# Performance work log

Hardware: AMD Instinct MI355X
Metric: run time of the kernel (lower is better)

## Reference

```python
import jax, jax.numpy as jnp
import numpy as np

IN_FEATURES = 2048
OUT_FEATURES = 2048
BATCH = 4096


def setup_inputs() -> dict:
    key = jax.random.key(0)
    kx, kw, kb, kp = jax.random.split(key, 4)
    x = jax.random.normal(kx, (BATCH, IN_FEATURES), dtype=jnp.float32)
    weight = jax.random.normal(kw, (OUT_FEATURES, IN_FEATURES), dtype=jnp.float32)
    bias = jax.random.normal(kb, (OUT_FEATURES,), dtype=jnp.float32)
    # torch uses torch.randperm(in_features) at forward time; we fix a permutation here
    indices = jax.random.permutation(kp, IN_FEATURES).astype(jnp.int64)
    return {"x": x, "weight": weight, "bias": bias, "indices": indices}


def reference(x, weight, bias, indices):
    # Original: (x[:, None, :] * weight)[:, :, indices].sum(dim=2) + bias
    # Summing the permuted reduction axis == contracting the permuted operands;
    # we gather both x and weight along the permutation then do a real GEMM,
    # avoiding the huge [B, out, in] intermediate while keeping identical math.
    xp = x[:, indices]            # [B, in]
    wp = weight[:, indices]       # [out, in]
    return jnp.einsum('bi,oi->bo', xp, wp) + bias[None, :]
```

## Files before the change

kernel.cpp:

```cpp
#include <hip/hip_runtime.h>
#include <hip/hip_bf16.h>

#define M_DIM 4096
#define N_DIM 2048
#define K_DIM 2048

#define BM 256
#define BN 128
#define BK 64
#define NT (K_DIM / BK)
#define A_TILE (BM * BK)
#define B_TILE (BN * BK)

typedef __bf16 bf16x8 __attribute__((ext_vector_type(8)));
typedef float f32x4 __attribute__((ext_vector_type(4)));
typedef unsigned short u16x8 __attribute__((ext_vector_type(8)));

__device__ __forceinline__ unsigned short f32_to_bf16_rne(float f) {
  unsigned int u = __float_as_uint(f);
  u += 0x7fffu + ((u >> 16) & 1u);
  return (unsigned short)(u >> 16);
}

__global__ __launch_bounds__(256) void cvt_both(
    const float* __restrict__ x, const float* __restrict__ w,
    unsigned short* __restrict__ out, int xn8, int totn8) {
  int i = blockIdx.x * 256 + threadIdx.x;
  if (i >= totn8) return;
  const float* src = (i < xn8) ? (x + (size_t)i * 8)
                               : (w + (size_t)(i - xn8) * 8);
  f32x4 a = reinterpret_cast<const f32x4*>(src)[0];
  f32x4 b = reinterpret_cast<const f32x4*>(src)[1];
  u16x8 o;
  o[0] = f32_to_bf16_rne(a[0]); o[1] = f32_to_bf16_rne(a[1]);
  o[2] = f32_to_bf16_rne(a[2]); o[3] = f32_to_bf16_rne(a[3]);
  o[4] = f32_to_bf16_rne(b[0]); o[5] = f32_to_bf16_rne(b[1]);
  o[6] = f32_to_bf16_rne(b[2]); o[7] = f32_to_bf16_rne(b[3]);
  reinterpret_cast<u16x8*>(out)[i] = o;
}

__device__ __forceinline__ void gload_lds16(const unsigned short* g, unsigned short* l) {
  __builtin_amdgcn_global_load_lds(
      (const __attribute__((address_space(1))) unsigned int*)g,
      (__attribute__((address_space(3))) unsigned int*)l, 16, 0, 0);
}

#define LD8(p) (*reinterpret_cast<const bf16x8*>(p))

__global__ __launch_bounds__(512, 2) void gemm_8w(
    const unsigned short* __restrict__ A,
    const unsigned short* __restrict__ B,
    const float* __restrict__ bias,
    float* __restrict__ C) {
  __shared__ unsigned short As[3 * A_TILE];
  __shared__ unsigned short Bs[3 * B_TILE];

  const int tid  = threadIdx.x;
  const int lane = tid & 63;
  const int wave = tid >> 6;
  const int wr   = wave >> 1;
  const int wc   = wave & 1;
  const int bn   = blockIdx.x;
  const int bm   = blockIdx.y;

  const int srow   = tid >> 3;
  const int schunk = (tid & 7) ^ (srow & 7);
  const unsigned short* Ag[4];
  const unsigned short* Bg[2];
#pragma unroll
  for (int j = 0; j < 4; ++j)
    Ag[j] = A + (size_t)(bm * BM + j * 64 + srow) * K_DIM + schunk * 8;
#pragma unroll
  for (int j = 0; j < 2; ++j)
    Bg[j] = B + (size_t)(bn * BN + j * 64 + srow) * K_DIM + schunk * 8;

#define STAGE_A01(buf, k0) do { \
    unsigned short* _d = &As[(buf) * A_TILE + tid * 8]; \
    gload_lds16(Ag[0] + (k0), _d); \
    gload_lds16(Ag[1] + (k0), _d + 4096); \
  } while (0)
#define STAGE_A23(buf, k0) do { \
    unsigned short* _d = &As[(buf) * A_TILE + 8192 + tid * 8]; \
    gload_lds16(Ag[2] + (k0), _d); \
    gload_lds16(Ag[3] + (k0), _d + 4096); \
  } while (0)
#define STAGE_B01(buf, k0) do { \
    unsigned short* _d = &Bs[(buf) * B_TILE + tid * 8]; \
    gload_lds16(Bg[0] + (k0), _d); \
    gload_lds16(Bg[1] + (k0), _d + 4096); \
  } while (0)

  const int fr = lane & 15;
  const int qq = lane >> 4;
  const int xr = fr & 7;
  int aoff[4][2], boff[4][2];
#pragma unroll
  for (int mi = 0; mi < 4; ++mi)
#pragma unroll
    for (int kk = 0; kk < 2; ++kk)
      aoff[mi][kk] = ((wr * 64 + mi * 16 + fr) * 8 + ((kk * 4 + qq) ^ xr)) * 8;
#pragma unroll
  for (int ni = 0; ni < 4; ++ni)
#pragma unroll
    for (int kk = 0; kk < 2; ++kk)
      boff[ni][kk] = ((wc * 64 + ni * 16 + fr) * 8 + ((kk * 4 + qq) ^ xr)) * 8;

  const f32x4 z = {0.f, 0.f, 0.f, 0.f};
  f32x4 acc[4][4];
#pragma unroll
  for (int i = 0; i < 4; ++i)
#pragma unroll
    for (int j = 0; j < 4; ++j) acc[i][j] = z;

#define MFMA_ROW(mi, av) do { \
    acc[mi][0] = __builtin_amdgcn_mfma_f32_16x16x32_bf16(av, bv0, acc[mi][0], 0, 0, 0); \
    acc[mi][1] = __builtin_amdgcn_mfma_f32_16x16x32_bf16(av, bv1, acc[mi][1], 0, 0, 0); \
    acc[mi][2] = __builtin_amdgcn_mfma_f32_16x16x32_bf16(av, bv2, acc[mi][2], 0, 0, 0); \
    acc[mi][3] = __builtin_amdgcn_mfma_f32_16x16x32_bf16(av, bv3, acc[mi][3], 0, 0, 0); \
  } while (0)

#define BODY(t_, STG) do { \
    const int b_ = (t_) % 3; \
    const unsigned short* Asb = &As[b_ * A_TILE]; \
    const unsigned short* Bsb = &Bs[b_ * B_TILE]; \
    const int sb_ = ((t_) + 2) % 3; \
    const int sk0_ = ((t_) + 2) * BK; \
    bf16x8 av0, av1, av2, av3, bv0, bv1, bv2, bv3; \
     \
    bv0 = LD8(Bsb + boff[0][0]); bv1 = LD8(Bsb + boff[1][0]); \
    bv2 = LD8(Bsb + boff[2][0]); bv3 = LD8(Bsb + boff[3][0]); \
    av0 = LD8(Asb + aoff[0][0]); av1 = LD8(Asb + aoff[1][0]); \
    if (STG) STAGE_A01(sb_, sk0_); \
    __builtin_amdgcn_s_setprio(1); \
    MFMA_ROW(0, av0); MFMA_ROW(1, av1); \
    __builtin_amdgcn_s_setprio(0); \
    av2 = LD8(Asb + aoff[2][0]); av3 = LD8(Asb + aoff[3][0]); \
    if (STG) STAGE_A23(sb_, sk0_); \
    __builtin_amdgcn_s_setprio(1); \
    MFMA_ROW(2, av2); MFMA_ROW(3, av3); \
    __builtin_amdgcn_s_setprio(0); \
     \
    bv0 = LD8(Bsb + boff[0][1]); bv1 = LD8(Bsb + boff[1][1]); \
    bv2 = LD8(Bsb + boff[2][1]); bv3 = LD8(Bsb + boff[3][1]); \
    av0 = LD8(Asb + aoff[0][1]); av1 = LD8(Asb + aoff[1][1]); \
    if (STG) STAGE_B01(sb_, sk0_); \
    __builtin_amdgcn_s_setprio(1); \
    MFMA_ROW(0, av0); MFMA_ROW(1, av1); \
    __builtin_amdgcn_s_setprio(0); \
    av2 = LD8(Asb + aoff[2][1]); av3 = LD8(Asb + aoff[3][1]); \
    __builtin_amdgcn_s_setprio(1); \
    MFMA_ROW(2, av2); MFMA_ROW(3, av3); \
    __builtin_amdgcn_s_setprio(0); \
  } while (0)

  STAGE_A01(0, 0); STAGE_A23(0, 0); STAGE_B01(0, 0);
  STAGE_A01(1, BK); STAGE_A23(1, BK); STAGE_B01(1, BK);
  asm volatile("s_waitcnt vmcnt(6)" ::: "memory");
  __builtin_amdgcn_s_barrier();
  __builtin_amdgcn_sched_barrier(0);

#pragma unroll 1
  for (int t = 0; t < NT - 2; ++t) {
    BODY(t, 1);
    asm volatile("s_waitcnt vmcnt(6)" ::: "memory");
    __builtin_amdgcn_s_barrier();
    __builtin_amdgcn_sched_barrier(0);
  }
  BODY(NT - 2, 0);
  asm volatile("s_waitcnt vmcnt(0)" ::: "memory");
  __builtin_amdgcn_s_barrier();
  __builtin_amdgcn_sched_barrier(0);
  BODY(NT - 1, 0);

  const int orow0 = bm * BM + wr * 64 + qq * 4;
  const int ocol0 = bn * BN + wc * 64 + fr;
#pragma unroll
  for (int ni = 0; ni < 4; ++ni) {
    const int col = ocol0 + ni * 16;
    const float bv = bias[col];
#pragma unroll
    for (int mi = 0; mi < 4; ++mi) {
      const int row = orow0 + mi * 16;
#pragma unroll
      for (int r = 0; r < 4; ++r)
        C[(size_t)(row + r) * N_DIM + col] = acc[mi][ni][r] + bv;
    }
  }
#undef BODY
#undef MFMA_ROW
#undef STAGE_A01
#undef STAGE_A23
#undef STAGE_B01
}

__global__ __launch_bounds__(256) void gemm_f32_naive(
    const float* __restrict__ X, const float* __restrict__ W,
    const float* __restrict__ bias, float* __restrict__ C) {
  int o = blockIdx.x * 256 + threadIdx.x;
  if (o >= M_DIM * N_DIM) return;
  int m = o / N_DIM, n = o % N_DIM;
  const float* xr = X + (size_t)m * K_DIM;
  const float* wr = W + (size_t)n * K_DIM;
  float s = 0.f;
  for (int k = 0; k < K_DIM; ++k) s += xr[k] * wr[k];
  C[o] = s + bias[n];
}

extern "C" void kernel_launch(void* const* d_in, const int* in_sizes, int n_in,
                              void* d_out, int out_size, void* d_ws, size_t ws_size,
                              hipStream_t stream) {
  const float* x    = (const float*)d_in[0];
  const float* w    = (const float*)d_in[1];
  const float* bias = (const float*)d_in[2];
  float* out = (float*)d_out;

  const size_t x_elems = (size_t)M_DIM * K_DIM;
  const size_t w_elems = (size_t)N_DIM * K_DIM;
  const size_t need = (x_elems + w_elems) * sizeof(unsigned short);

  if (ws_size < need) {
    gemm_f32_naive<<<(M_DIM * N_DIM + 255) / 256, 256, 0, stream>>>(x, w, bias, out);
    return;
  }

  unsigned short* xb = (unsigned short*)d_ws;
  unsigned short* wb = xb + x_elems;

  const int xn8 = (int)(x_elems / 8);
  const int totn8 = (int)((x_elems + w_elems) / 8);
  cvt_both<<<(totn8 + 255) / 256, 256, 0, stream>>>(x, w, xb, xn8, totn8);

  dim3 grid(N_DIM / BN, M_DIM / BM);
  gemm_8w<<<grid, 512, 0, stream>>>(xb, wb, bias, out);
}
```

Measured before the change: 62.09 us.

## Restructure K-loop into two barrier-synchronized load/MFMA phases per tile

Each K-tile iteration is reorganized into two halves. In each half, all LDS fragment reads and global-to-LDS staging are issued first, then the block hits a barrier and waits on lgkmcnt, then 16 MFMAs run back-to-back. This replaces the earlier interleaving of loads and MFMAs within a half. The goal is to keep all waves in lockstep, ping-pong style, so memory and matrix phases from co-resident blocks overlap and MFMA bursts are longer. It adds several extra barriers per tile and removes intra-wave overlap of LDS reads with MFMAs, which risks stalls.

```diff
diff --git a/kernel.cpp b/kernel.cpp
--- a/kernel.cpp
+++ b/kernel.cpp
@@ -119,7 +119,12 @@
     acc[mi][3] = __builtin_amdgcn_mfma_f32_16x16x32_bf16(av, bv3, acc[mi][3], 0, 0, 0); \
   } while (0)
 
-#define BODY(t_, STG) do { \
+#define TRAIL_WAIT(W) do { \
+    if ((W) == 6)      asm volatile("s_waitcnt vmcnt(6)" ::: "memory"); \
+    else if ((W) == 0) asm volatile("s_waitcnt vmcnt(0)" ::: "memory"); \
+  } while (0)
+
+#define TILE(t_, STG, W) do { \
     const int b_ = (t_) % 3; \
     const unsigned short* Asb = &As[b_ * A_TILE]; \
     const unsigned short* Bsb = &Bs[b_ * B_TILE]; \
@@ -130,27 +135,29 @@
     bv0 = LD8(Bsb + boff[0][0]); bv1 = LD8(Bsb + boff[1][0]); \
     bv2 = LD8(Bsb + boff[2][0]); bv3 = LD8(Bsb + boff[3][0]); \
     av0 = LD8(Asb + aoff[0][0]); av1 = LD8(Asb + aoff[1][0]); \
-    if (STG) STAGE_A01(sb_, sk0_); \
+    av2 = LD8(Asb + aoff[2][0]); av3 = LD8(Asb + aoff[3][0]); \
+    if (STG) { STAGE_A01(sb_, sk0_); STAGE_A23(sb_, sk0_); } \
+    __builtin_amdgcn_s_barrier(); \
+    asm volatile("s_waitcnt lgkmcnt(0)" ::: "memory"); \
+    __builtin_amdgcn_sched_barrier(0); \
     __builtin_amdgcn_s_setprio(1); \
-    MFMA_ROW(0, av0); MFMA_ROW(1, av1); \
+    MFMA_ROW(0, av0); MFMA_ROW(1, av1); MFMA_ROW(2, av2); MFMA_ROW(3, av3); \
     __builtin_amdgcn_s_setprio(0); \
-    av2 = LD8(Asb + aoff[2][0]); av3 = LD8(Asb + aoff[3][0]); \
-    if (STG) STAGE_A23(sb_, sk0_); \
-    __builtin_amdgcn_s_setprio(1); \
-    MFMA_ROW(2, av2); MFMA_ROW(3, av3); \
-    __builtin_amdgcn_s_setprio(0); \
+    __builtin_amdgcn_s_barrier(); \
      \
     bv0 = LD8(Bsb + boff[0][1]); bv1 = LD8(Bsb + boff[1][1]); \
     bv2 = LD8(Bsb + boff[2][1]); bv3 = LD8(Bsb + boff[3][1]); \
     av0 = LD8(Asb + aoff[0][1]); av1 = LD8(Asb + aoff[1][1]); \
+    av2 = LD8(Asb + aoff[2][1]); av3 = LD8(Asb + aoff[3][1]); \
     if (STG) STAGE_B01(sb_, sk0_); \
+    __builtin_amdgcn_s_barrier(); \
+    asm volatile("s_waitcnt lgkmcnt(0)" ::: "memory"); \
+    __builtin_amdgcn_sched_barrier(0); \
     __builtin_amdgcn_s_setprio(1); \
-    MFMA_ROW(0, av0); MFMA_ROW(1, av1); \
+    MFMA_ROW(0, av0); MFMA_ROW(1, av1); MFMA_ROW(2, av2); MFMA_ROW(3, av3); \
     __builtin_amdgcn_s_setprio(0); \
-    av2 = LD8(Asb + aoff[2][1]); av3 = LD8(Asb + aoff[3][1]); \
-    __builtin_amdgcn_s_setprio(1); \
-    MFMA_ROW(2, av2); MFMA_ROW(3, av3); \
-    __builtin_amdgcn_s_setprio(0); \
+    TRAIL_WAIT(W); \
+    __builtin_amdgcn_s_barrier(); \
   } while (0)
 
   STAGE_A01(0, 0); STAGE_A23(0, 0); STAGE_B01(0, 0);
@@ -161,16 +168,10 @@
 
 #pragma unroll 1
   for (int t = 0; t < NT - 2; ++t) {
-    BODY(t, 1);
-    asm volatile("s_waitcnt vmcnt(6)" ::: "memory");
-    __builtin_amdgcn_s_barrier();
-    __builtin_amdgcn_sched_barrier(0);
+    TILE(t, 1, 6);
   }
-  BODY(NT - 2, 0);
-  asm volatile("s_waitcnt vmcnt(0)" ::: "memory");
-  __builtin_amdgcn_s_barrier();
-  __builtin_amdgcn_sched_barrier(0);
-  BODY(NT - 1, 0);
+  TILE(NT - 2, 0, 0);
+  TILE(NT - 1, 0, -1);
 
   const int orow0 = bm * BM + wr * 64 + qq * 4;
   const int ocol0 = bn * BN + wc * 64 + fr;
@@ -186,7 +187,8 @@
         C[(size_t)(row + r) * N_DIM + col] = acc[mi][ni][r] + bv;
     }
   }
-#undef BODY
+#undef TILE
+#undef TRAIL_WAIT
 #undef MFMA_ROW
 #undef STAGE_A01
 #undef STAGE_A23
```

Result: slower. 64.23 us (+3.4%).

## Software-pipeline LDS fragment reads across k-halves with double register sets

Applied to the files above, without the earlier changes.

Restructures the GEMM main loop so the LDS fragment reads for the next k-half (or next tile) are issued into a second register set while the MFMAs of the current set run. The loop is unrolled by three to make buffer indices compile-time, and all global-to-LDS staging is issued at once at the start of each tile. The aim is to hide LDS read latency behind MFMA work. The cost is more VGPRs for the duplicated fragments, plus an extra barrier per tile, which could pressure occupancy at 2 blocks per CU.

```diff
diff --git a/kernel.cpp b/kernel.cpp
--- a/kernel.cpp
+++ b/kernel.cpp
@@ -46,6 +46,10 @@
 }
 
 #define LD8(p) (*reinterpret_cast<const bf16x8*>(p))
+#define VMWAIT_(n) asm volatile("s_waitcnt vmcnt(" #n ")" ::: "memory")
+#define VMWAIT(n) VMWAIT_(n)
+#define SBAR() __builtin_amdgcn_s_barrier()
+#define SCHED() __builtin_amdgcn_sched_barrier(0)
 
 __global__ __launch_bounds__(512, 2) void gemm_8w(
     const unsigned short* __restrict__ A,
@@ -74,20 +78,15 @@
   for (int j = 0; j < 2; ++j)
     Bg[j] = B + (size_t)(bn * BN + j * 64 + srow) * K_DIM + schunk * 8;
 
-#define STAGE_A01(buf, k0) do { \
-    unsigned short* _d = &As[(buf) * A_TILE + tid * 8]; \
-    gload_lds16(Ag[0] + (k0), _d); \
-    gload_lds16(Ag[1] + (k0), _d + 4096); \
-  } while (0)
-#define STAGE_A23(buf, k0) do { \
-    unsigned short* _d = &As[(buf) * A_TILE + 8192 + tid * 8]; \
-    gload_lds16(Ag[2] + (k0), _d); \
-    gload_lds16(Ag[3] + (k0), _d + 4096); \
-  } while (0)
-#define STAGE_B01(buf, k0) do { \
-    unsigned short* _d = &Bs[(buf) * B_TILE + tid * 8]; \
-    gload_lds16(Bg[0] + (k0), _d); \
-    gload_lds16(Bg[1] + (k0), _d + 4096); \
+#define STAGE_ALL(buf, k0) do { \
+    unsigned short* _da = &As[(buf) * A_TILE + tid * 8]; \
+    unsigned short* _db = &Bs[(buf) * B_TILE + tid * 8]; \
+    gload_lds16(Ag[0] + (k0), _da); \
+    gload_lds16(Ag[1] + (k0), _da + 4096); \
+    gload_lds16(Ag[2] + (k0), _da + 8192); \
+    gload_lds16(Ag[3] + (k0), _da + 12288); \
+    gload_lds16(Bg[0] + (k0), _db); \
+    gload_lds16(Bg[1] + (k0), _db + 4096); \
   } while (0)
 
   const int fr = lane & 15;
@@ -112,65 +111,75 @@
 #pragma unroll
     for (int j = 0; j < 4; ++j) acc[i][j] = z;
 
-#define MFMA_ROW(mi, av) do { \
-    acc[mi][0] = __builtin_amdgcn_mfma_f32_16x16x32_bf16(av, bv0, acc[mi][0], 0, 0, 0); \
-    acc[mi][1] = __builtin_amdgcn_mfma_f32_16x16x32_bf16(av, bv1, acc[mi][1], 0, 0, 0); \
-    acc[mi][2] = __builtin_amdgcn_mfma_f32_16x16x32_bf16(av, bv2, acc[mi][2], 0, 0, 0); \
-    acc[mi][3] = __builtin_amdgcn_mfma_f32_16x16x32_bf16(av, bv3, acc[mi][3], 0, 0, 0); \
-  } while (0)
-
-#define BODY(t_, STG) do { \
-    const int b_ = (t_) % 3; \
-    const unsigned short* Asb = &As[b_ * A_TILE]; \
-    const unsigned short* Bsb = &Bs[b_ * B_TILE]; \
-    const int sb_ = ((t_) + 2) % 3; \
-    const int sk0_ = ((t_) + 2) * BK; \
-    bf16x8 av0, av1, av2, av3, bv0, bv1, bv2, bv3; \
-     \
-    bv0 = LD8(Bsb + boff[0][0]); bv1 = LD8(Bsb + boff[1][0]); \
-    bv2 = LD8(Bsb + boff[2][0]); bv3 = LD8(Bsb + boff[3][0]); \
-    av0 = LD8(Asb + aoff[0][0]); av1 = LD8(Asb + aoff[1][0]); \
-    if (STG) STAGE_A01(sb_, sk0_); \
+  bf16x8 avA[4], bvA[4], avB[4], bvB[4];
+
+#define READ_SET(av, bv, bufi, kk) do { \
+    const unsigned short* Asb = &As[(bufi) * A_TILE]; \
+    const unsigned short* Bsb = &Bs[(bufi) * B_TILE]; \
+    bv[0] = LD8(Bsb + boff[0][kk]); bv[1] = LD8(Bsb + boff[1][kk]); \
+    bv[2] = LD8(Bsb + boff[2][kk]); bv[3] = LD8(Bsb + boff[3][kk]); \
+    av[0] = LD8(Asb + aoff[0][kk]); av[1] = LD8(Asb + aoff[1][kk]); \
+    av[2] = LD8(Asb + aoff[2][kk]); av[3] = LD8(Asb + aoff[3][kk]); \
+  } while (0)
+
+#define MFMA_ALL(av, bv) do { \
     __builtin_amdgcn_s_setprio(1); \
-    MFMA_ROW(0, av0); MFMA_ROW(1, av1); \
+    _Pragma("unroll") \
+    for (int mi = 0; mi < 4; ++mi) { \
+      acc[mi][0] = __builtin_amdgcn_mfma_f32_16x16x32_bf16(av[mi], bv[0], acc[mi][0], 0, 0, 0); \
+      acc[mi][1] = __builtin_amdgcn_mfma_f32_16x16x32_bf16(av[mi], bv[1], acc[mi][1], 0, 0, 0); \
+      acc[mi][2] = __builtin_amdgcn_mfma_f32_16x16x32_bf16(av[mi], bv[2], acc[mi][2], 0, 0, 0); \
+      acc[mi][3] = __builtin_amdgcn_mfma_f32_16x16x32_bf16(av[mi], bv[3], acc[mi][3], 0, 0, 0); \
+    } \
     __builtin_amdgcn_s_setprio(0); \
-    av2 = LD8(Asb + aoff[2][0]); av3 = LD8(Asb + aoff[3][0]); \
-    if (STG) STAGE_A23(sb_, sk0_); \
-    __builtin_amdgcn_s_setprio(1); \
-    MFMA_ROW(2, av2); MFMA_ROW(3, av3); \
-    __builtin_amdgcn_s_setprio(0); \
-     \
-    bv0 = LD8(Bsb + boff[0][1]); bv1 = LD8(Bsb + boff[1][1]); \
-    bv2 = LD8(Bsb + boff[2][1]); bv3 = LD8(Bsb + boff[3][1]); \
-    av0 = LD8(Asb + aoff[0][1]); av1 = LD8(Asb + aoff[1][1]); \
-    if (STG) STAGE_B01(sb_, sk0_); \
-    __builtin_amdgcn_s_setprio(1); \
-    MFMA_ROW(0, av0); MFMA_ROW(1, av1); \
-    __builtin_amdgcn_s_setprio(0); \
-    av2 = LD8(Asb + aoff[2][1]); av3 = LD8(Asb + aoff[3][1]); \
-    __builtin_amdgcn_s_setprio(1); \
-    MFMA_ROW(2, av2); MFMA_ROW(3, av3); \
-    __builtin_amdgcn_s_setprio(0); \
-  } while (0)
-
-  STAGE_A01(0, 0); STAGE_A23(0, 0); STAGE_B01(0, 0);
-  STAGE_A01(1, BK); STAGE_A23(1, BK); STAGE_B01(1, BK);
-  asm volatile("s_waitcnt vmcnt(6)" ::: "memory");
-  __builtin_amdgcn_s_barrier();
-  __builtin_amdgcn_sched_barrier(0);
+  } while (0)
+
+#define TILE_MAIN(bufi, stgbufi, stgt) do { \
+    STAGE_ALL(stgbufi, (stgt) * BK); \
+    READ_SET(avB, bvB, bufi, 1); \
+    SCHED(); \
+    MFMA_ALL(avA, bvA); \
+    SCHED(); \
+    VMWAIT(6); \
+    SBAR(); \
+    SCHED(); \
+    READ_SET(avA, bvA, ((bufi) + 1) % 3, 0); \
+    SCHED(); \
+    MFMA_ALL(avB, bvB); \
+    SBAR(); \
+    SCHED(); \
+  } while (0)
+
+  STAGE_ALL(0, 0);
+  STAGE_ALL(1, BK);
+  VMWAIT(6);
+  SBAR();
+  SCHED();
+  READ_SET(avA, bvA, 0, 0);
+  SCHED();
 
 #pragma unroll 1
-  for (int t = 0; t < NT - 2; ++t) {
-    BODY(t, 1);
-    asm volatile("s_waitcnt vmcnt(6)" ::: "memory");
-    __builtin_amdgcn_s_barrier();
-    __builtin_amdgcn_sched_barrier(0);
+  for (int s = 0; s < 10; ++s) {
+    const int t0 = s * 3;
+    TILE_MAIN(0, 2, t0 + 2);
+    TILE_MAIN(1, 0, t0 + 3);
+    TILE_MAIN(2, 1, t0 + 4);
   }
-  BODY(NT - 2, 0);
-  asm volatile("s_waitcnt vmcnt(0)" ::: "memory");
-  __builtin_amdgcn_s_barrier();
-  __builtin_amdgcn_sched_barrier(0);
-  BODY(NT - 1, 0);
+
+  READ_SET(avB, bvB, 0, 1);
+  SCHED();
+  MFMA_ALL(avA, bvA);
+  SCHED();
+  VMWAIT(0);
+  SBAR();
+  SCHED();
+  READ_SET(avA, bvA, 1, 0);
+  SCHED();
+  MFMA_ALL(avB, bvB);
+  READ_SET(avB, bvB, 1, 1);
+  SCHED();
+  MFMA_ALL(avA, bvA);
+  MFMA_ALL(avB, bvB);
 
   const int orow0 = bm * BM + wr * 64 + qq * 4;
   const int ocol0 = bn * BN + wc * 64 + fr;
@@ -186,11 +195,10 @@
         C[(size_t)(row + r) * N_DIM + col] = acc[mi][ni][r] + bv;
     }
   }
-#undef BODY
-#undef MFMA_ROW
-#undef STAGE_A01
-#undef STAGE_A23
-#undef STAGE_B01
+#undef TILE_MAIN
+#undef MFMA_ALL
+#undef READ_SET
+#undef STAGE_ALL
 }
 
 __global__ __launch_bounds__(256) void gemm_f32_naive(
```

After: 55.52 us. 10.6% less time.
